# Kernel tuning notes

Measured on AMD Instinct MI355X. Metric: run time of the kernel, lower is better.

The kernel has to match this reference:

```python
import jax, jax.numpy as jnp
import numpy as np

N_NODES = 50000
N_EDGES = 400000
IN_DIM = 256
OUT_DIM = 64
HEADS = 2
ATTN_HIDDEN = 64
ALPHA = 0.2
TEMP = 0.55


def setup_inputs() -> dict:
    key = jax.random.key(0)
    k_x, k_src, k_dst, k_w, k_wa, k_a = jax.random.split(key, 6)
    x = jax.random.normal(k_x, (N_NODES, IN_DIM), dtype=jnp.float32)
    src = jax.random.randint(k_src, (N_EDGES,), 0, N_NODES, dtype=jnp.int32)
    dst = jnp.sort(jax.random.randint(k_dst, (N_EDGES,), 0, N_NODES, dtype=jnp.int32))
    # Glorot-uniform-like params
    def glorot(k, shape, fan_in, fan_out):
        lim = jnp.sqrt(6.0 / (fan_in + fan_out))
        return jax.random.uniform(k, shape, jnp.float32, -lim, lim)
    W = glorot(k_w, (IN_DIM, HEADS, OUT_DIM), IN_DIM, HEADS * OUT_DIM)
    W_attn = glorot(k_wa, (HEADS, 2 * OUT_DIM, ATTN_HIDDEN), 2 * OUT_DIM, ATTN_HIDDEN)
    a_vec = glorot(k_a, (HEADS, ATTN_HIDDEN), HEADS, ATTN_HIDDEN)
    return {"x": x, "W": W, "W_attn": W_attn, "a_vec": a_vec, "src": src, "dst": dst}


def reference(x, W, W_attn, a_vec, src, dst):
    N = x.shape[0]
    # node-level projection: [N, H, F]
    Wh = jnp.einsum('nd,dhf->nhf', x, W)
    # per-edge gathers
    Wh_src = Wh[src]                                   # [E, H, F]
    Wh_dst = Wh[dst]                                   # [E, H, F]
    z = jnp.concatenate([Wh_src, Wh_dst], axis=-1)     # [E, H, 2F]
    z_act = jax.nn.leaky_relu(jnp.einsum('ehf,hfc->ehc', z, W_attn), ALPHA)
    logits = jnp.einsum('ehc,hc->eh', z_act, a_vec).astype(jnp.float32) / TEMP
    # per-head segment softmax over incoming edges of each dst node
    seg_max = jax.ops.segment_max(logits, dst, num_segments=N)   # [N, H]
    ex = jnp.exp(logits - seg_max[dst])
    seg_sum = jax.ops.segment_sum(ex, dst, num_segments=N)
    alphas = (ex / (seg_sum[dst] + 1e-9)).astype(Wh_src.dtype)   # [E, H]
    # weighted scatter-sum of source messages
    out = jax.ops.segment_sum(Wh_src * alphas[..., None], dst, num_segments=N)  # [N, H, F]
    # concat=False -> mean over heads (dropout is identity at inference)
    return out.mean(axis=1)
```

## Files before the change

### kernel.cpp

```cpp
#include <hip/hip_runtime.h>
#include <hip/hip_bf16.h>
#include <math.h>

#define N_NODES 50000
#define N_EDGES 400000
#define IN_DIM 256
#define OUT_DIM 64
#define HEADS 2
#define ATTN_HIDDEN 64
#define ALPHA_SLOPE 0.2f
#define TEMP 0.55f
#define NHF 128
#define ZDIM 384

typedef __bf16 bf16x8 __attribute__((ext_vector_type(8)));
typedef float f32x4 __attribute__((ext_vector_type(4)));

__device__ __forceinline__ ushort f2bf(float f) {
    unsigned u = __float_as_uint(f);
    u = (u + 0x7fffu + ((u >> 16) & 1u)) >> 16;
    return (ushort)u;
}
__device__ __forceinline__ unsigned pack2(float a, float b) {
    return (unsigned)f2bf(a) | ((unsigned)f2bf(b) << 16);
}
__device__ __forceinline__ float bfl(unsigned u) { return __uint_as_float(u << 16); }
__device__ __forceinline__ float bfh(unsigned u) { return __uint_as_float(u & 0xffff0000u); }

__global__ __launch_bounds__(256) void k_combine(const float* __restrict__ W,
                                                 const float* __restrict__ Wa,
                                                 ushort* __restrict__ Wct) {
    __shared__ float col[64];
    const int n = blockIdx.x;
    const int t = threadIdx.x;
    if (n < 128) {
        Wct[(size_t)n * 256 + t] = f2bf(W[(size_t)t * NHF + n]);
        return;
    }
    const int part = (n - 128) >> 7;
    const int idx = (n - 128) & 127;
    const int h = idx >> 6;
    const int c = idx & 63;
    const int fb = part ? 64 : 0;
    if (t < 64) col[t] = Wa[(size_t)h * 8192 + (size_t)(fb + t) * 64 + c];
    __syncthreads();
    const float* wr = W + (size_t)t * NHF + h * 64;
    float acc = 0.f;
#pragma unroll
    for (int f = 0; f < 64; f++) acc += wr[f] * col[f];
    Wct[(size_t)n * 256 + t] = f2bf(acc);
}

__global__ void k_segstart(const int* __restrict__ dst, int* __restrict__ seg) {
    int n = blockIdx.x * blockDim.x + threadIdx.x;
    if (n > N_NODES) return;
    int lo = 0, hi = N_EDGES;
    while (lo < hi) {
        int mid = (lo + hi) >> 1;
        if (dst[mid] < n) lo = mid + 1; else hi = mid;
    }
    seg[n] = lo;
}

#define LDT 40
__global__ __launch_bounds__(256) void k_gemm(const float* __restrict__ x,
                                              const ushort* __restrict__ Wct,
                                              ushort* __restrict__ Zb) {
    __shared__ ushort As[64 * LDT];
    __shared__ ushort Bs[384 * LDT];
    const int t = threadIdx.x;
    const int w = t >> 6, lane = t & 63;
    const int q = lane >> 4, r16 = lane & 15;
    const int row0 = blockIdx.x * 64;

    f32x4 acc[24];
#pragma unroll
    for (int c = 0; c < 24; c++) acc[c] = (f32x4){0.f, 0.f, 0.f, 0.f};

    const int arow = t >> 2, a8 = (t & 3) * 8;
    const int agrow = row0 + arow;

    for (int k0 = 0; k0 < IN_DIM; k0 += 32) {
        float4 v0 = make_float4(0.f, 0.f, 0.f, 0.f), v1 = v0;
        if (agrow < N_NODES) {
            const float* xp = x + (size_t)agrow * IN_DIM + k0 + a8;
            v0 = *(const float4*)xp;
            v1 = *(const float4*)(xp + 4);
        }
        uint4 av;
        av.x = pack2(v0.x, v0.y); av.y = pack2(v0.z, v0.w);
        av.z = pack2(v1.x, v1.y); av.w = pack2(v1.z, v1.w);
        *(uint4*)(As + arow * LDT + a8) = av;
#pragma unroll
        for (int i = 0; i < 6; i++) {
            int brow = (t >> 2) + 64 * i;
            uint4 bv = *(const uint4*)(Wct + (size_t)brow * 256 + k0 + a8);
            *(uint4*)(Bs + brow * LDT + a8) = bv;
        }
        __syncthreads();
        bf16x8 af = *(const bf16x8*)(As + (w * 16 + r16) * LDT + q * 8);
#pragma unroll
        for (int c = 0; c < 24; c++) {
            bf16x8 bf = *(const bf16x8*)(Bs + (c * 16 + r16) * LDT + q * 8);
            acc[c] = __builtin_amdgcn_mfma_f32_16x16x32_bf16(af, bf, acc[c], 0, 0, 0);
        }
        __syncthreads();
    }
#pragma unroll
    for (int c = 0; c < 24; c++) {
#pragma unroll
        for (int rr = 0; rr < 4; rr++) {
            int row = row0 + w * 16 + q * 4 + rr;
            if (row < N_NODES)
                Zb[(size_t)row * ZDIM + c * 16 + r16] = f2bf(acc[c][rr]);
        }
    }
}

__global__ __launch_bounds__(256) void k_fused(const ushort* __restrict__ Zb,
                                               const float* __restrict__ avec,
                                               const int* __restrict__ src,
                                               const int* __restrict__ seg,
                                               float* __restrict__ out) {
    const int wv = threadIdx.x >> 6;
    const int lane = threadIdx.x & 63;
    const int n = blockIdx.x * 4 + wv;
    if (n >= N_NODES) return;
    const int h = lane >> 5, cp = lane & 31;
    const int choff = h * 64 + 2 * cp;

    const float2 a2 = *(const float2*)(avec + choff);
    const unsigned ud = *(const unsigned*)(Zb + (size_t)n * ZDIM + 256 + choff);
    const float udl = bfl(ud), udh = bfh(ud);

    const int e0 = seg[n], e1 = seg[n + 1];
    float m = -INFINITY, l = 0.f, acc0 = 0.f, acc1 = 0.f;

    unsigned us = 0, wh = 0;
    if (e0 < e1) {
        const int s = src[e0];
        us = *(const unsigned*)(Zb + (size_t)s * ZDIM + 128 + choff);
        wh = *(const unsigned*)(Zb + (size_t)s * ZDIM + choff);
    }
    for (int e = e0; e < e1; e++) {
        const unsigned cus = us, cwh = wh;
        if (e + 1 < e1) {
            const int sn = src[e + 1];
            us = *(const unsigned*)(Zb + (size_t)sn * ZDIM + 128 + choff);
            wh = *(const unsigned*)(Zb + (size_t)sn * ZDIM + choff);
        }
        float v0 = bfl(cus) + udl, v1 = bfh(cus) + udh;
        v0 = v0 > 0.f ? v0 : ALPHA_SLOPE * v0;
        v1 = v1 > 0.f ? v1 : ALPHA_SLOPE * v1;
        float p = v0 * a2.x + v1 * a2.y;
        p += __shfl_xor(p, 1, 64);
        p += __shfl_xor(p, 2, 64);
        p += __shfl_xor(p, 4, 64);
        p += __shfl_xor(p, 8, 64);
        p += __shfl_xor(p, 16, 64);
        const float logit = p * (1.0f / TEMP);
        const float nm = fmaxf(m, logit);
        const float sc = __expf(m - nm);
        const float wgt = __expf(logit - nm);
        l = l * sc + wgt;
        acc0 = acc0 * sc + wgt * bfl(cwh);
        acc1 = acc1 * sc + wgt * bfh(cwh);
        m = nm;
    }
    const float inv = 1.f / (l + 1e-9f);
    float ax = acc0 * inv, ay = acc1 * inv;
    ax += __shfl_xor(ax, 32, 64);
    ay += __shfl_xor(ay, 32, 64);
    if (lane < 32) {
        float2 o = make_float2(0.5f * ax, 0.5f * ay);
        *(float2*)(out + (size_t)n * 64 + 2 * cp) = o;
    }
}

extern "C" void kernel_launch(void* const* d_in, const int* in_sizes, int n_in,
                              void* d_out, int out_size, void* d_ws, size_t ws_size,
                              hipStream_t stream) {
    const float* x    = (const float*)d_in[0];
    const float* W    = (const float*)d_in[1];
    const float* Wa   = (const float*)d_in[2];
    const float* avec = (const float*)d_in[3];
    const int*   src  = (const int*)d_in[4];
    const int*   dst  = (const int*)d_in[5];
    float* out = (float*)d_out;

    ushort* Zb  = (ushort*)d_ws;
    ushort* Wct = Zb + 19200000;
    int*    seg = (int*)((char*)d_ws + 38596608);

    k_combine <<<ZDIM, 256, 0, stream>>>(W, Wa, Wct);
    k_segstart<<<(N_NODES + 1 + 255) / 256, 256, 0, stream>>>(dst, seg);
    k_gemm    <<<(N_NODES + 63) / 64, 256, 0, stream>>>(x, Wct, Zb);
    k_fused   <<<(N_NODES + 3) / 4, 256, 0, stream>>>(Zb, avec, src, seg, out);
}
```

Baseline: 190.7 us.

## Process four nodes per wavefront with 16-byte vector gathers in fused edge kernel

The fused softmax-aggregation kernel now assigns 16 lanes per destination node instead of a whole 64-lane wavefront. Each lane loads 8 bf16 channels with one uint4 gather rather than 2 channels with a 32-bit load. The per-edge reduction shrinks to three shuffles, and the head-mean uses a single xor-8 shuffle. This cuts per-edge instruction and shuffle overhead and raises bytes per memory request, at the cost of more registers per lane and more divergence from unequal segment lengths within a wave.

```diff
diff --git a/kernel.cpp b/kernel.cpp
--- a/kernel.cpp
+++ b/kernel.cpp
@@ -122,58 +122,84 @@
                                                const int* __restrict__ src,
                                                const int* __restrict__ seg,
                                                float* __restrict__ out) {
+    const int lane = threadIdx.x & 63;
     const int wv = threadIdx.x >> 6;
-    const int lane = threadIdx.x & 63;
-    const int n = blockIdx.x * 4 + wv;
+    const int g = lane >> 4, l16 = lane & 15;
+    const int n = blockIdx.x * 16 + wv * 4 + g;
     if (n >= N_NODES) return;
-    const int h = lane >> 5, cp = lane & 31;
-    const int choff = h * 64 + 2 * cp;
-
-    const float2 a2 = *(const float2*)(avec + choff);
-    const unsigned ud = *(const unsigned*)(Zb + (size_t)n * ZDIM + 256 + choff);
-    const float udl = bfl(ud), udh = bfh(ud);
+    const int choff = 8 * l16;
+
+    const float4 af0 = *(const float4*)(avec + choff);
+    const float4 af1 = *(const float4*)(avec + choff + 4);
+    const float a[8] = {af0.x, af0.y, af0.z, af0.w, af1.x, af1.y, af1.z, af1.w};
+
+    const uint4 udv = *(const uint4*)(Zb + (size_t)n * ZDIM + 256 + choff);
+    const float ud[8] = {bfl(udv.x), bfh(udv.x), bfl(udv.y), bfh(udv.y),
+                         bfl(udv.z), bfh(udv.z), bfl(udv.w), bfh(udv.w)};
 
     const int e0 = seg[n], e1 = seg[n + 1];
-    float m = -INFINITY, l = 0.f, acc0 = 0.f, acc1 = 0.f;
-
-    unsigned us = 0, wh = 0;
+    float m = -INFINITY, l = 0.f;
+    float acc[8] = {0.f, 0.f, 0.f, 0.f, 0.f, 0.f, 0.f, 0.f};
+
+    uint4 us = make_uint4(0, 0, 0, 0), wh = us;
     if (e0 < e1) {
         const int s = src[e0];
-        us = *(const unsigned*)(Zb + (size_t)s * ZDIM + 128 + choff);
-        wh = *(const unsigned*)(Zb + (size_t)s * ZDIM + choff);
+        us = *(const uint4*)(Zb + (size_t)s * ZDIM + 128 + choff);
+        wh = *(const uint4*)(Zb + (size_t)s * ZDIM + choff);
     }
     for (int e = e0; e < e1; e++) {
-        const unsigned cus = us, cwh = wh;
+        const uint4 cus = us, cwh = wh;
         if (e + 1 < e1) {
             const int sn = src[e + 1];
-            us = *(const unsigned*)(Zb + (size_t)sn * ZDIM + 128 + choff);
-            wh = *(const unsigned*)(Zb + (size_t)sn * ZDIM + choff);
-        }
-        float v0 = bfl(cus) + udl, v1 = bfh(cus) + udh;
-        v0 = v0 > 0.f ? v0 : ALPHA_SLOPE * v0;
-        v1 = v1 > 0.f ? v1 : ALPHA_SLOPE * v1;
-        float p = v0 * a2.x + v1 * a2.y;
+            us = *(const uint4*)(Zb + (size_t)sn * ZDIM + 128 + choff);
+            wh = *(const uint4*)(Zb + (size_t)sn * ZDIM + choff);
+        }
+        float p;
+        {
+            float v0, v1, s0, s1;
+            v0 = bfl(cus.x) + ud[0]; v1 = bfh(cus.x) + ud[1];
+            s0 = fmaxf(v0, ALPHA_SLOPE * v0); s1 = fmaxf(v1, ALPHA_SLOPE * v1);
+            p = s0 * a[0] + s1 * a[1];
+            v0 = bfl(cus.y) + ud[2]; v1 = bfh(cus.y) + ud[3];
+            s0 = fmaxf(v0, ALPHA_SLOPE * v0); s1 = fmaxf(v1, ALPHA_SLOPE * v1);
+            p += s0 * a[2] + s1 * a[3];
+            v0 = bfl(cus.z) + ud[4]; v1 = bfh(cus.z) + ud[5];
+            s0 = fmaxf(v0, ALPHA_SLOPE * v0); s1 = fmaxf(v1, ALPHA_SLOPE * v1);
+            p += s0 * a[4] + s1 * a[5];
+            v0 = bfl(cus.w) + ud[6]; v1 = bfh(cus.w) + ud[7];
+            s0 = fmaxf(v0, ALPHA_SLOPE * v0); s1 = fmaxf(v1, ALPHA_SLOPE * v1);
+            p += s0 * a[6] + s1 * a[7];
+        }
         p += __shfl_xor(p, 1, 64);
         p += __shfl_xor(p, 2, 64);
         p += __shfl_xor(p, 4, 64);
-        p += __shfl_xor(p, 8, 64);
-        p += __shfl_xor(p, 16, 64);
         const float logit = p * (1.0f / TEMP);
         const float nm = fmaxf(m, logit);
         const float sc = __expf(m - nm);
         const float wgt = __expf(logit - nm);
         l = l * sc + wgt;
-        acc0 = acc0 * sc + wgt * bfl(cwh);
-        acc1 = acc1 * sc + wgt * bfh(cwh);
+        acc[0] = acc[0] * sc + wgt * bfl(cwh.x);
+        acc[1] = acc[1] * sc + wgt * bfh(cwh.x);
+        acc[2] = acc[2] * sc + wgt * bfl(cwh.y);
+        acc[3] = acc[3] * sc + wgt * bfh(cwh.y);
+        acc[4] = acc[4] * sc + wgt * bfl(cwh.z);
+        acc[5] = acc[5] * sc + wgt * bfh(cwh.z);
+        acc[6] = acc[6] * sc + wgt * bfl(cwh.w);
+        acc[7] = acc[7] * sc + wgt * bfh(cwh.w);
         m = nm;
     }
-    const float inv = 1.f / (l + 1e-9f);
-    float ax = acc0 * inv, ay = acc1 * inv;
-    ax += __shfl_xor(ax, 32, 64);
-    ay += __shfl_xor(ay, 32, 64);
-    if (lane < 32) {
-        float2 o = make_float2(0.5f * ax, 0.5f * ay);
-        *(float2*)(out + (size_t)n * 64 + 2 * cp) = o;
+    const float inv = 0.5f / (l + 1e-9f);
+#pragma unroll
+    for (int j = 0; j < 8; j++) {
+        const float v = acc[j] * inv;
+        acc[j] = v + __shfl_xor(v, 8, 64);
+    }
+    if (l16 < 8) {
+        float4 o0 = make_float4(acc[0], acc[1], acc[2], acc[3]);
+        float4 o1 = make_float4(acc[4], acc[5], acc[6], acc[7]);
+        float* op = out + (size_t)n * 64 + choff;
+        *(float4*)op = o0;
+        *(float4*)(op + 4) = o1;
     }
 }
 
@@ -195,5 +221,5 @@
     k_combine <<<ZDIM, 256, 0, stream>>>(W, Wa, Wct);
     k_segstart<<<(N_NODES + 1 + 255) / 256, 256, 0, stream>>>(dst, seg);
     k_gemm    <<<(N_NODES + 63) / 64, 256, 0, stream>>>(x, Wct, Zb);
-    k_fused   <<<(N_NODES + 3) / 4, 256, 0, stream>>>(Zb, avec, src, seg, out);
-}
+    k_fused   <<<(N_NODES + 15) / 16, 256, 0, stream>>>(Zb, avec, src, seg, out);
+}
```

After: 169.1 us. 1.13x faster.
